# Optimization experiments

Measured on AMD Instinct MI355X. Metric: run time of the kernel, lower is better.

The kernel has to match this reference:

```python
import jax, jax.numpy as jnp
import numpy as np

NEG_SLOPE_GAT = 0.2   # GATConv internal leaky_relu slope (PyG default)
NEG_SLOPE = 0.01      # nn.LeakyReLU default slope


def _gat(h_src_in, h_dst_in, src, dst, Wsrc, Wdst, a_s, a_d, b, n_dst, self_loops):
    """Single-head PyG-style GATConv: gather -> score -> edge softmax -> scatter-sum."""
    hs = h_src_in @ Wsrc            # [N_src, C]
    hd = h_dst_in @ Wdst            # [N_dst, C]
    if self_loops:                  # static flag; same node set on both sides
        loop = jnp.arange(n_dst, dtype=src.dtype)
        src = jnp.concatenate([src, loop])
        dst = jnp.concatenate([dst, loop])
    # attention logits per edge
    e = jax.nn.leaky_relu((hs @ a_s)[src] + (hd @ a_d)[dst], NEG_SLOPE_GAT)  # [E]
    # softmax over edges sharing a destination node
    m = jax.ops.segment_max(e, dst, num_segments=n_dst)
    ex = jnp.exp(e - m[dst])
    denom = jax.ops.segment_sum(ex, dst, num_segments=n_dst)
    alpha = ex / denom[dst]
    out = jax.ops.segment_sum(hs[src] * alpha[:, None], dst, num_segments=n_dst)
    return out + b


def setup_inputs() -> dict:
    key = jax.random.key(0)
    ks = iter(jax.random.split(key, 64))
    NB, NP = 100_000, 50_000
    E_bb, E_pp, E_bp = 800_000, 400_000, 400_000
    FB, FP, H, H2 = 32, 34, 64, 32
    rn = lambda shape, s=0.05: jax.random.normal(next(ks), shape, jnp.float32) * s
    d = {}
    d['x_b'] = rn((NB, FB), 1.0)
    d['x_p'] = rn((NP, FP), 1.0)
    d['ei_bb'] = jax.random.randint(next(ks), (2, E_bb), 0, NB, jnp.int32)
    d['ei_pp'] = jax.random.randint(next(ks), (2, E_pp), 0, NP, jnp.int32)
    d['ei_bp_src'] = jax.random.randint(next(ks), (E_bp,), 0, NB, jnp.int32)
    d['ei_bp_dst'] = jax.random.randint(next(ks), (E_bp,), 0, NP, jnp.int32)
    d['W_in_b'] = rn((FB, H)); d['b_in_b'] = jnp.zeros((H,), jnp.float32)
    d['W_in_p'] = rn((FP, H)); d['b_in_p'] = jnp.zeros((H,), jnp.float32)
    for tag, cin, cout in (('1', H, H), ('2', H, H2)):
        d['W_bb' + tag] = rn((cin, cout)); d['as_bb' + tag] = rn((cout,)); d['ad_bb' + tag] = rn((cout,)); d['b_bb' + tag] = jnp.zeros((cout,), jnp.float32)
        d['W_pp' + tag] = rn((cin, cout)); d['as_pp' + tag] = rn((cout,)); d['ad_pp' + tag] = rn((cout,)); d['b_pp' + tag] = jnp.zeros((cout,), jnp.float32)
        d['Ws_bp' + tag] = rn((cin, cout)); d['Wd_bp' + tag] = rn((cin, cout)); d['as_bp' + tag] = rn((cout,)); d['ad_bp' + tag] = rn((cout,)); d['b_bp' + tag] = jnp.zeros((cout,), jnp.float32)
    d['W_out'] = rn((H2, 1)); d['b_out'] = jnp.zeros((1,), jnp.float32)
    return d


def reference(x_b, x_p, ei_bb, ei_pp, ei_bp_src, ei_bp_dst,
              W_in_b, b_in_b, W_in_p, b_in_p,
              W_bb1, as_bb1, ad_bb1, b_bb1, W_pp1, as_pp1, ad_pp1, b_pp1,
              Ws_bp1, Wd_bp1, as_bp1, ad_bp1, b_bp1,
              W_bb2, as_bb2, ad_bb2, b_bb2, W_pp2, as_pp2, ad_pp2, b_pp2,
              Ws_bp2, Wd_bp2, as_bp2, ad_bp2, b_bp2,
              W_out, b_out):
    NB, NP = x_b.shape[0], x_p.shape[0]
    lr = lambda v: jax.nn.leaky_relu(v, NEG_SLOPE)
    # input projections (dropout is eval-mode identity)
    hb = lr(x_b @ W_in_b + b_in_b)
    hp = lr(x_p @ W_in_p + b_in_p)
    # hetero conv 1 (sum aggregation over relations sharing a dst type)
    ob = _gat(hb, hb, ei_bb[0], ei_bb[1], W_bb1, W_bb1, as_bb1, ad_bb1, b_bb1, NB, True)
    op = (_gat(hp, hp, ei_pp[0], ei_pp[1], W_pp1, W_pp1, as_pp1, ad_pp1, b_pp1, NP, True)
          + _gat(hb, hp, ei_bp_src, ei_bp_dst, Ws_bp1, Wd_bp1, as_bp1, ad_bp1, b_bp1, NP, False))
    hb, hp = lr(ob), lr(op)
    # hetero conv 2
    ob2 = _gat(hb, hb, ei_bb[0], ei_bb[1], W_bb2, W_bb2, as_bb2, ad_bb2, b_bb2, NB, True)
    op2 = (_gat(hp, hp, ei_pp[0], ei_pp[1], W_pp2, W_pp2, as_pp2, ad_pp2, b_pp2, NP, True)
           + _gat(hb, hp, ei_bp_src, ei_bp_dst, Ws_bp2, Wd_bp2, as_bp2, ad_bp2, b_bp2, NP, False))
    hp = lr(op2)
    return hp @ W_out + b_out  # [NP, 1]
```

## Files before the change

kernel.cpp:

```cpp
#include <hip/hip_runtime.h>
#include <hip/hip_bf16.h>
#include <cstdint>
#include <cstddef>


typedef __attribute__((ext_vector_type(8))) short short8;
typedef __attribute__((ext_vector_type(4))) float f32x4;
typedef unsigned int u32;
typedef __hip_bfloat16 bf16;

#define ABITS 9
#define CHUNKE 4096

static __device__ __forceinline__ float b2f(bf16 v) { return __bfloat162float(v); }

static __device__ __forceinline__ float ldf(const void* p, int i, int bf) {
    return bf ? __bfloat162float(((const bf16*)p)[i]) : ((const float*)p)[i];
}

static __device__ __forceinline__ short f2bs(float f) {
    bf16 h = __float2bfloat16(f);
    return *reinterpret_cast<short*>(&h);
}
static __device__ __forceinline__ float bs2f(short s) {
    bf16 h = *reinterpret_cast<bf16*>(&s);
    return __bfloat162float(h);
}
static __device__ __forceinline__ float lo16(u32 u) { return bs2f((short)(u & 0xffffu)); }
static __device__ __forceinline__ float hi16(u32 u) { return bs2f((short)(u >> 16)); }
// ... 16 lines not shown
        c += (e >= 100u && e <= 145u) ? 1 : 0;
    }
    atomicAdd(cnt, c);
    __syncthreads();
    int r = (*cnt > 614) ? 1 : 0;
    __syncthreads();
    return r;
}

__global__ __launch_bounds__(256) void k_fv(
    const unsigned* __restrict__ probe_w, int* __restrict__ flag,
    const void* W_bb1, const void* as_bb1, const void* ad_bb1,
    const void* Ws_bp1, const void* as_bp1,
    const void* W_pp1, const void* as_pp1, const void* ad_pp1,
    const void* Wd_bp1, const void* ad_bp1,
    float* __restrict__ FVg)
{
    __shared__ int cnt;
    int bf = probe_bf(probe_w, &cnt);
    if (threadIdx.x == 0) *flag = bf;
    int lane = threadIdx.x & 63, wv = threadIdx.x >> 6;
    const void* Ws[6] = { W_bb1, W_bb1, Ws_bp1, W_pp1, W_pp1, Wd_bp1 };
    const void* av[6] = { as_bb1, ad_bb1, as_bp1, as_pp1, ad_pp1, ad_bp1 };
#pragma unroll
    for (int v = 0; v < 6; ++v) {
        float a = ldf(av[v], lane, bf);
        for (int k = wv; k < 64; k += 4) {
            float p = ldf(Ws[v], k * 64 + lane, bf) * a;
#pragma unroll
            for (int off = 1; off < 64; off <<= 1) p += __shfl_xor(p, off);
            if (lane == 0) FVg[v * 64 + k] = p;
        }
    }
// ... 77 lines not shown
            vs[r] += __shfl_xor(vs[r], off);
            vd[r] += __shfl_xor(vd[r], off);
            ve[r] += __shfl_xor(ve[r], off);
        }
    int c = lane & 15;
    int row = row0 + quad * 4 + (c & 3);
    if (row < M && c < 12) {
        if (c < 4)       S0[row]  = sel4(vs, c & 3);
        else if (c < 8)  S1v[row] = sel4(vd, c & 3);
        else             S2v[row] = sel4(ve, c & 3);
    }
}

__global__ __launch_bounds__(256) void k_hist_inproj(
    const int* __restrict__ bb_d, const int* __restrict__ pp_d,
    const int* __restrict__ bp_d, int* __restrict__ histM,
    const unsigned* __restrict__ probe_w, int* __restrict__ flag,
    int E_bb, int E_pp, int E_bp, int NB, int NP, int nbkt, int nblk,
    const void* __restrict__ Xb, const void* __restrict__ Wb, const void* __restrict__ Bb,
    bf16* __restrict__ Yb, int MB,
    const void* __restrict__ Xp, const void* __restrict__ Wp, const void* __restrict__ Bp,
    bf16* __restrict__ Yp, int MP,
    const float* __restrict__ FVg,
    float* __restrict__ ss_bb, float* __restrict__ sd_bb, float* __restrict__ ss_bp,
    float* __restrict__ ss_pp, float* __restrict__ sd_pp, float* __restrict__ sd_bp)
{
    __shared__ short WT[64 * 40];
    __shared__ float bl[64];
    __shared__ float FV[192];
    __shared__ int aux[1 << ABITS];
    if ((int)blockIdx.x < nblk) {
        for (int i = threadIdx.x; i < nbkt; i += 256) aux[i] = 0;
        __syncthreads();
        int E_all = E_bb + E_pp + E_bp;
        int base = blockIdx.x * CHUNKE;
        int end = base + CHUNKE < E_all ? base + CHUNKE : E_all;
        for (int i = base + threadIdx.x; i < end; i += 256) {
            int d;
            if (i < E_bb) d = bb_d[i];
            else if (i < E_bb + E_pp) d = NB + pp_d[i - E_bb];
            else d = NB + NP + bp_d[i - E_bb - E_pp];
            atomicAdd(&aux[d >> ABITS], 1);
        }
        __syncthreads();
        for (int i = threadIdx.x; i < nbkt; i += 256)
            histM[(size_t)i * nblk + blockIdx.x] = aux[i];
    } else {
        int bfv = probe_bf(probe_w, &aux[0]);
        int bid = blockIdx.x - nblk;
        int nbb = (MB + 63) >> 6;
        if (bid < nbb)
            in_proj_body<32>(WT, bl, FV, bid, Xb, Wb, Bb, FVg,
                Yb, ss_bb, sd_bb, ss_bp, MB, bfv);
        else
            in_proj_body<34>(WT, bl, FV, bid - nbb, Xp, Wp, Bp, FVg + 192,
                Yp, ss_pp, sd_pp, sd_bp, MP, bfv);
    }
}

__global__ __launch_bounds__(1024) void k_scan1(const int* __restrict__ deg,
                                                int* __restrict__ out,
                                                int* __restrict__ bsum, int n)
{
// ... 41 lines not shown
    if (wid == 0 && lane < 16) {
        int w0 = wsum[lane];
#pragma unroll
        for (int off = 1; off < 16; off <<= 1) {
            int y = __shfl_up(w0, off, 16);
            if (lane >= off) w0 += y;
        }
        wsum[lane] = w0;
    }
    __syncthreads();
    int base = (wid > 0) ? wsum[wid - 1] : 0;
    if (threadIdx.x < nb) bsum[threadIdx.x] = base + x - v;
}

__global__ __launch_bounds__(1024) void k_scan3(int* __restrict__ indptr,
                                                const int* __restrict__ bsum,
                                                int n, int E)
{
    int gid = blockIdx.x * 1024 + threadIdx.x;
    if (gid < n) indptr[gid] += bsum[blockIdx.x];
    if (gid == 0) indptr[n] = E;
}

template <int N1, int N2, bool S1F, bool S2F>
static __device__ __forceinline__ void dual_body(
    short* WT, int bid, const bf16* __restrict__ H,
    const void* __restrict__ W1, const void* __restrict__ W2,
    const void* __restrict__ as1, const void* __restrict__ ad1,
    const void* __restrict__ as2, const void* __restrict__ ad2,
    bf16* __restrict__ HS1, bf16* __restrict__ HS2,
    float* __restrict__ SS1, float* __restrict__ SD1,
    float* __restrict__ SS2, float* __restrict__ SD2,
    int M, int bf)
{
    constexpr int KP = 72;
    constexpr int T1 = N1 / 16, T2 = N2 / 16, T = T1 + T2;
    for (int i = threadIdx.x; i < N1 * 64; i += 256) {
        int n = i >> 6, k = i & 63;
        WT[n * KP + k] = f2bs(ldf(W1, k * N1 + n, bf));
    }
    for (int i = threadIdx.x; i < N2 * 64; i += 256) {
        int n = i >> 6, k = i & 63;
        WT[(N1 + n) * KP + k] = f2bs(ldf(W2, k * N2 + n, bf));
    }
    __syncthreads();

    int lane = threadIdx.x & 63;
    int wv   = threadIdx.x >> 6;
    int m = lane & 15, quad = lane >> 4;
    int row0 = (bid * 4 + wv) * 16;
    if (row0 >= M) return;

    const short* Hs = (const short*)H;
    int arow = row0 + m; if (arow >= M) arow = M - 1;

    f32x4 acc[T] = {};
#pragma unroll
    for (int ks = 0; ks < 2; ++ks) {
        short8 a = *(const short8*)&Hs[(size_t)arow * 64 + ks * 32 + quad * 8];
#pragma unroll
        for (int tt = 0; tt < T; ++tt) {
            short8 bfr = *(const short8*)&WT[((lane & 15) + 16 * tt) * KP + ks * 32 + quad * 8];
            acc[tt] = __builtin_amdgcn_mfma_f32_16x16x32_bf16(a, bfr, acc[tt], 0, 0, 0);
        }
    }

    float vs1[4] = {}, vd1[4] = {}, vs2[4] = {}, vd2[4] = {};
#pragma unroll
    for (int tt = 0; tt < T1; ++tt) {
        int col = (lane & 15) + 16 * tt;
        float av = ldf(as1, col, bf), dv = ldf(ad1, col, bf);
#pragma unroll
        for (int r = 0; r < 4; ++r) {
            vs1[r] += acc[tt][r] * av;
            vd1[r] += acc[tt][r] * dv;
        }
    }
#pragma unroll
    for (int tt = 0; tt < T2; ++tt) {
        int col = (lane & 15) + 16 * tt;
        float av = ldf(as2, col, bf), dv = ldf(ad2, col, bf);
#pragma unroll
        for (int r = 0; r < 4; ++r) {
            vs2[r] += acc[T1 + tt][r] * av;
            vd2[r] += acc[T1 + tt][r] * dv;
        }
    }
#pragma unroll
    for (int off = 1; off < 16; off <<= 1)
#pragma unroll
        for (int r = 0; r < 4; ++r) {
            vs1[r] += __shfl_xor(vs1[r], off);
            vd1[r] += __shfl_xor(vd1[r], off);
            vs2[r] += __shfl_xor(vs2[r], off);
            vd2[r] += __shfl_xor(vd2[r], off);
        }
    int c = lane & 15;
    {
        int row = row0 + quad * 4 + (c & 3);
        if (row < M) {
            if (c < 4)       SS1[row] = sel4(vs1, c & 3);
            else if (c < 8)  SD1[row] = sel4(vd1, c & 3);
            else if (c < 12) SS2[row] = sel4(vs2, c & 3);
            else             SD2[row] = sel4(vd2, c & 3);
        }
    }

    if (S1F) {
#pragma unroll
        for (int tt = 0; tt < T1; ++tt) {
            int col = (lane & 15) + 16 * tt;
#pragma unroll
            for (int r = 0; r < 4; ++r) {
                int row = row0 + quad * 4 + r;
                if (row < M)
                    HS1[(size_t)row * N1 + col] = __float2bfloat16(acc[tt][r]);
            }
        }
    }
    if (S2F) {
#pragma unroll
        for (int tt = 0; tt < T2; ++tt) {
            int col = (lane & 15) + 16 * tt;
#pragma unroll
            for (int r = 0; r < 4; ++r) {
                int row = row0 + quad * 4 + r;
                if (row < M)
                    HS2[(size_t)row * N2 + col] = __float2bfloat16(acc[T1 + tt][r]);
            }
        }
    }
}

template <int N, bool STORE>
static __device__ __forceinline__ void proj_body(
    short* WT, int bid, const bf16* __restrict__ H, const void* __restrict__ W,
    const void* __restrict__ a_s, const void* __restrict__ a_d,
    bf16* __restrict__ HS, float* __restrict__ SS, float* __restrict__ SD,
    int M, int bf)
{
    constexpr int KP = 72;
    constexpr int T = N / 16;
    for (int i = threadIdx.x; i < N * 64; i += 256) {
        int n = i >> 6, k = i & 63;
        WT[n * KP + k] = f2bs(ldf(W, k * N + n, bf));
    }
    __syncthreads();

    int lane = threadIdx.x & 63;
    int wv   = threadIdx.x >> 6;
    int m = lane & 15, quad = lane >> 4;
    int row0 = (bid * 4 + wv) * 16;
    if (row0 >= M) return;

    const short* Hs = (const short*)H;
    int arow = row0 + m; if (arow >= M) arow = M - 1;

    f32x4 acc[T] = {};
#pragma unroll
    for (int ks = 0; ks < 2; ++ks) {
        short8 a = *(const short8*)&Hs[(size_t)arow * 64 + ks * 32 + quad * 8];
#pragma unroll
        for (int tt = 0; tt < T; ++tt) {
            short8 bfr = *(const short8*)&WT[((lane & 15) + 16 * tt) * KP + ks * 32 + quad * 8];
            acc[tt] = __builtin_amdgcn_mfma_f32_16x16x32_bf16(a, bfr, acc[tt], 0, 0, 0);
        }
    }

    float asv[T], adv[T];
#pragma unroll
    for (int tt = 0; tt < T; ++tt) {
        int col = (lane & 15) + 16 * tt;
        asv[tt] = ldf(a_s, col, bf);
        adv[tt] = ldf(a_d, col, bf);
    }
    float vs[4] = {}, vd[4] = {};
#pragma unroll
    for (int tt = 0; tt < T; ++tt)
#pragma unroll
        for (int r = 0; r < 4; ++r) {
            vs[r] += acc[tt][r] * asv[tt];
            vd[r] += acc[tt][r] * adv[tt];
        }
#pragma unroll
    for (int off = 1; off < 16; off <<= 1)
#pragma unroll
        for (int r = 0; r < 4; ++r) {
            vs[r] += __shfl_xor(vs[r], off);
            vd[r] += __shfl_xor(vd[r], off);
        }
    int c = lane & 15;
    if (c < 8) {
        int row = row0 + quad * 4 + (c & 3);
        if (row < M) {
            if (c < 4) SS[row] = sel4(vs, c & 3);
            else       SD[row] = sel4(vd, c & 3);
        }
    }

    if (STORE) {
#pragma unroll
        for (int tt = 0; tt < T; ++tt) {
            int col = (lane & 15) + 16 * tt;
#pragma unroll
            for (int r = 0; r < 4; ++r) {
                int row = row0 + quad * 4 + r;
                if (row < M)
                    HS[(size_t)row * N + col] = __float2bfloat16(acc[tt][r]);
            }
        }
    }
}

__global__ __launch_bounds__(256) void k_scatter(
    const int* __restrict__ bb_s, const int* __restrict__ bb_d,
    const int* __restrict__ pp_s, const int* __restrict__ pp_d,
    const int* __restrict__ bp_s, const int* __restrict__ bp_d,
    const int* __restrict__ histS, unsigned* __restrict__ ebuf,
    int E_bb, int E_pp, int E_bp, int NB, int NP, int nbkt, int nblk)
{
    __shared__ int cur[1 << ABITS];
    for (int i = threadIdx.x; i < nbkt; i += 256)
        cur[i] = histS[(size_t)i * nblk + blockIdx.x];
    __syncthreads();
    int E_all = E_bb + E_pp + E_bp;
    int base = blockIdx.x * CHUNKE;
    int end = base + CHUNKE < E_all ? base + CHUNKE : E_all;
    for (int i = base + threadIdx.x; i < end; i += 256) {
        int s, d;
        if (i < E_bb) { s = bb_s[i]; d = bb_d[i]; }
        else if (i < E_bb + E_pp) { int j = i - E_bb; s = pp_s[j]; d = NB + pp_d[j]; }
        else { int j = i - E_bb - E_pp; s = bp_s[j]; d = NB + NP + bp_d[j]; }
        int p = atomicAdd(&cur[d >> ABITS], 1);
        ebuf[p] = ((unsigned)(d & ((1 << ABITS) - 1)) << 20) | (unsigned)s;
    }
}

__global__ __launch_bounds__(256) void k_finalize(
    const unsigned* __restrict__ ebuf, const int* __restrict__ histS,
    int* __restrict__ ip_all, int2* __restrict__ sw,
    const float* __restrict__ ss_bb, const float* __restrict__ sd_bb,
    const float* __restrict__ ss_pp, const float* __restrict__ sd_pp,
    const float* __restrict__ ss_bp, const float* __restrict__ sd_bp,
    int NB, int NP, int NALL, int E_all, int nbkt, int nblk)
{
    __shared__ int h[1 << ABITS];
    __shared__ int pre[1 << ABITS];
    __shared__ int wq[4];
    int b = blockIdx.x;
    int d0 = b << ABITS;
    int nloc = NALL - d0 < (1 << ABITS) ? NALL - d0 : (1 << ABITS);
    int t = threadIdx.x;
    for (int i = t; i < (1 << ABITS); i += 256) h[i] = 0;
    __syncthreads();
    int s0 = histS[(size_t)b * nblk];
    int s1 = histS[(size_t)(b + 1) * nblk];
    for (int i = s0 + t; i < s1; i += 256)
        atomicAdd(&h[ebuf[i] >> 20], 1);
    __syncthreads();
    int v0 = h[2 * t], v1 = h[2 * t + 1];
    int ps = v0 + v1;
    int lane = t & 63, wid = t >> 6;
    int x = ps;
#pragma unroll
    for (int off = 1; off < 64; off <<= 1) {
        int y = __shfl_up(x, off, 64);
        if (lane >= off) x += y;
    }
    if (lane == 63) wq[wid] = x;
    __syncthreads();
    if (t == 0) {
        int a = 0;
#pragma unroll
        for (int w = 0; w < 4; ++w) { int tmp = wq[w]; wq[w] = a; a += tmp; }
    }
    __syncthreads();
    int excl = wq[wid] + x - ps;
    pre[2 * t]     = excl;
    pre[2 * t + 1] = excl + v0;
    __syncthreads();
    for (int i = t; i < nloc; i += 256) ip_all[d0 + i] = s0 + pre[i];
    if (d0 + nloc == NALL && t == 0) ip_all[NALL] = E_all;
    for (int i = t; i < (1 << ABITS); i += 256) h[i] = s0 + pre[i];
    __syncthreads();
    for (int i = s0 + t; i < s1; i += 256) {
        unsigned e = ebuf[i];
        int dl = (int)(e >> 20);
        int src = (int)(e & 0xFFFFFu);
        int p = atomicAdd(&h[dl], 1);
        int d = d0 + dl;
        float ssv, sdv;
        if (d < NB)           { ssv = ss_bb[src]; sdv = sd_bb[d]; }
        else if (d < NB + NP) { ssv = ss_pp[src]; sdv = sd_pp[d - NB]; }
        else                  { ssv = ss_bp[src]; sdv = sd_bp[d - NB - NP]; }
        int2 pk; pk.x = src; pk.y = __float_as_int(__expf(lrelu2(ssv + sdv)));
        sw[p] = pk;
    }
}

static __device__ __forceinline__ void gather1_body(
    int bid, const int* __restrict__ ip, const int2* __restrict__ sw,
    const float* __restrict__ SS, const float* __restrict__ SD,
    const bf16* __restrict__ HS, bf16* __restrict__ OUT, int M)
{
    int lane = threadIdx.x & 63;
    int half = lane >> 5, hl = lane & 31;
    int d = bid * 4 + (threadIdx.x >> 6);
    if (d >= M) return;
    const u32* H32 = (const u32*)HS;
    float ax = 0.f, ay = 0.f, den = 0.f;
// ... 104 lines not shown
    const float* __restrict__ ss_bb, const float* __restrict__ sd_bb,
    const bf16* __restrict__ hb, bf16* __restrict__ agg_bb, int NB,
    const int* __restrict__ ip_pp, const int* __restrict__ ip_bp,
    const float* __restrict__ ss_pp, const float* __restrict__ sd_pp,
    const bf16* __restrict__ hp,
    bf16* __restrict__ agg_pp, bf16* __restrict__ agg_bp, int NP)
{
    int nbb = (NB + 3) >> 2;
    if ((int)blockIdx.x < nbb)
        gather1_body(blockIdx.x, ip_bb, sw, ss_bb, sd_bb, hb, agg_bb, NB);
    else
        gather2_body(blockIdx.x - nbb, ip_pp, sw, ss_pp, sd_pp, hp,
                     ip_bp, hb, agg_pp, agg_bp, NP);
}

template <bool DUAL>
static __device__ __forceinline__ void postproj_body(
    short* WT, float* bl, int bid,
    const bf16* __restrict__ A1, const bf16* __restrict__ A2,
    const void* __restrict__ W1, const void* __restrict__ W2,
    const void* __restrict__ B1, const void* __restrict__ B2,
    bf16* __restrict__ OUT, int M, int bf)
{
    constexpr int KP = 72;
    for (int i = threadIdx.x; i < 64 * 64; i += 256) {
        int n = i >> 6, k = i & 63;
        WT[n * KP + k] = f2bs(ldf(W1, k * 64 + n, bf));
        if (DUAL) WT[(64 + n) * KP + k] = f2bs(ldf(W2, k * 64 + n, bf));
    }
    if (threadIdx.x < 64) {
        float b = ldf(B1, threadIdx.x, bf);
        if (DUAL) b += ldf(B2, threadIdx.x, bf);
        bl[threadIdx.x] = b;
    }
    __syncthreads();

    int lane = threadIdx.x & 63;
    int wv   = threadIdx.x >> 6;
    int m = lane & 15, quad = lane >> 4;
    int row0 = (bid * 4 + wv) * 16;
    if (row0 >= M) return;

    const short* A1s = (const short*)A1;
    const short* A2s = (const short*)A2;
    int arow = row0 + m; if (arow >= M) arow = M - 1;

    f32x4 acc[4] = {};
#pragma unroll
    for (int ks = 0; ks < 2; ++ks) {
        short8 a1 = *(const short8*)&A1s[(size_t)arow * 64 + ks * 32 + quad * 8];
#pragma unroll
        for (int tt = 0; tt < 4; ++tt) {
            short8 bfr = *(const short8*)&WT[((lane & 15) + 16 * tt) * KP + ks * 32 + quad * 8];
            acc[tt] = __builtin_amdgcn_mfma_f32_16x16x32_bf16(a1, bfr, acc[tt], 0, 0, 0);
        }
        if (DUAL) {
            short8 a2 = *(const short8*)&A2s[(size_t)arow * 64 + ks * 32 + quad * 8];
#pragma unroll
            for (int tt = 0; tt < 4; ++tt) {
                short8 bfr = *(const short8*)&WT[(64 + (lane & 15) + 16 * tt) * KP + ks * 32 + quad * 8];
                acc[tt] = __builtin_amdgcn_mfma_f32_16x16x32_bf16(a2, bfr, acc[tt], 0, 0, 0);
            }
        }
    }

#pragma unroll
    for (int tt = 0; tt < 4; ++tt) {
        int col = (lane & 15) + 16 * tt;
        float bb = bl[col];
#pragma unroll
        for (int r = 0; r < 4; ++r) {
            int row = row0 + quad * 4 + r;
            if (row < M) {
                float v = acc[tt][r] + bb;
                v = v > 0.f ? v : 0.01f * v;
                OUT[(size_t)row * 64 + col] = __float2bfloat16(v);
            }
        }
    }
}

__global__ __launch_bounds__(256) void k_postproj1(
    const bf16* __restrict__ agg_pp, const bf16* __restrict__ agg_bp,
    const void* W_pp1, const void* Ws_bp1,
    const void* b_pp1, const void* b_bp1, bf16* __restrict__ hp2, int MP,
    const bf16* __restrict__ agg_bb, const void* W_bb1, const void* b_bb1,
    bf16* __restrict__ hb2, int MB, const int* __restrict__ flag)
{
    const int bf = *flag;
    __shared__ short WT[128 * 72];
    __shared__ float bl[64];
    int npb = (MP + 63) >> 6;
    if ((int)blockIdx.x < npb)
        postproj_body<true>(WT, bl, blockIdx.x, agg_pp, agg_bp,
                            W_pp1, Ws_bp1, b_pp1, b_bp1, hp2, MP, bf);
    else
        postproj_body<false>(WT, bl, blockIdx.x - npb, agg_bb, nullptr,
                             W_bb1, nullptr, b_bb1, nullptr, hb2, MB, bf);
}

__global__ __launch_bounds__(256) void k_proj2_all(
    const bf16* __restrict__ hp2,
    const void* W_pp2, const void* Wd_bp2,
    const void* as_pp2, const void* ad_pp2, const void* as_bp2, const void* ad_bp2,
    bf16* hs2_pp, float* ss2_pp, float* sd2_pp, float* junkNP, float* sd2_bp, int MP,
    const bf16* __restrict__ hb2,
    const void* Ws_bp2, bf16* hs2_bp, float* ss2_bp, float* junkNB, int MB,
    const int* __restrict__ flag)
{
    const int bf = *flag;
    __shared__ short WT[64 * 72];
    int npb = (MP + 63) >> 6;
    if ((int)blockIdx.x < npb)
        dual_body<32, 32, true, false>(WT, blockIdx.x, hp2, W_pp2, Wd_bp2,
            as_pp2, ad_pp2, as_bp2, ad_bp2, hs2_pp, nullptr,
            ss2_pp, sd2_pp, junkNP, sd2_bp, MP, bf);
    else
        proj_body<32, true>(WT, blockIdx.x - npb, hb2, Ws_bp2,
            as_bp2, ad_bp2, hs2_bp, ss2_bp, junkNB, MB, bf);
}

__global__ __launch_bounds__(256) void k_gather_out(
    const int* __restrict__ ip1, const int2* __restrict__ sw,
    const float* __restrict__ SS1, const float* __restrict__ SD1,
    const bf16* __restrict__ HS1,
    const int* __restrict__ ip2,
    const float* __restrict__ SS2, const float* __restrict__ SD2,
    const bf16* __restrict__ HS2,
    const void* __restrict__ b1, const void* __restrict__ b2,
    const void* __restrict__ Wout, const void* __restrict__ bout,
    void* __restrict__ OUT, int M, const int* __restrict__ flag)
{
    const int bf = *flag;
    int lane = threadIdx.x & 63;
// ... 84 lines not shown
    const void *W_pp2 = d_in[27], *as_pp2 = d_in[28], *ad_pp2 = d_in[29], *b_pp2 = d_in[30];
    const void *Ws_bp2 = d_in[31], *Wd_bp2 = d_in[32], *as_bp2 = d_in[33], *ad_bp2 = d_in[34], *b_bp2 = d_in[35];
    const void *W_out = d_in[36], *b_out = d_in[37];

    const int NB   = in_sizes[0] / 32;
    const int NP   = in_sizes[1] / 34;
    const int E_bb = in_sizes[2] / 2;
    const int E_pp = in_sizes[3] / 2;
    const int E_bp = in_sizes[4];
    const int E_all = E_bb + E_pp + E_bp;
    const int NALL  = NB + 2 * NP;
    const int* bb_s = ei_bb;  const int* bb_d = ei_bb + E_bb;
    const int* pp_s = ei_pp;  const int* pp_d = ei_pp + E_pp;
    (void)ws_size; (void)n_in; (void)out_size;

    const int nbkt  = (NALL + (1 << ABITS) - 1) >> ABITS;
    const int nblk  = (E_all + CHUNKE - 1) / CHUNKE;
    const int nh    = nbkt * nblk;

    char* base = (char*)d_ws;
    size_t o = 0;
    auto alloc = [&](size_t bytes) { char* p = base + o; o += (bytes + 255) & ~(size_t)255; return p; };

    int* flag  = (int*)alloc(256);
    float* FVg = (float*)alloc(6 * 64 * 4);
    int* bsum  = (int*)alloc(1024 * 4);
    int* histM = (int*)alloc((size_t)nh * 4);
    int* histS = (int*)alloc((size_t)(nh + 1) * 4);
    int* ip_all = (int*)alloc((size_t)(NALL + 1) * 4);
    unsigned* ebuf = (unsigned*)alloc((size_t)E_all * 4);
    int2* sw = (int2*)alloc((size_t)E_all * 8);
    float* ss_bb = (float*)alloc((size_t)NB * 4);
    float* sd_bb = (float*)alloc((size_t)NB * 4);
    float* ss_bp = (float*)alloc((size_t)NB * 4);
    float* ss_pp = (float*)alloc((size_t)NP * 4);
    float* sd_pp = (float*)alloc((size_t)NP * 4);
    float* sd_bp = (float*)alloc((size_t)NP * 4);
    float* junkNB = (float*)alloc((size_t)NB * 4);
    float* junkNP = (float*)alloc((size_t)NP * 4);
    float* ss2_bp = ss_bb;
    float* ss2_pp = ss_pp;
    float* sd2_pp = sd_pp;
    float* sd2_bp = sd_bp;

    char* S1 = alloc((size_t)NB * 64 * 2);
    char* S2 = alloc((size_t)NP * 64 * 2);
    char* S3 = alloc((size_t)NB * 64 * 2);
    char* S4 = alloc((size_t)NB * 64 * 2);
    char* S5 = alloc((size_t)NB * 64 * 2);
    char* S6 = alloc((size_t)NP * 64 * 2);

    bf16* hb     = (bf16*)S1;
    bf16* hp     = (bf16*)S2;
    bf16* agg_bb = (bf16*)S3;
    bf16* hb2    = (bf16*)S4;
    bf16* agg_bp = (bf16*)S5;
    bf16* agg_pp = (bf16*)S6;
    bf16* hp2    = (bf16*)S2;
    bf16* hs2_pp = (bf16*)S3;
    bf16* hs2_bp = (bf16*)S1;

    auto cdiv = [](int a, int b) { return (a + b - 1) / b; };

    const int* ip_bb = ip_all;
    const int* ip_pp = ip_all + NB;
    const int* ip_bp = ip_all + NB + NP;

    k_fv<<<1, 256, 0, stream>>>(
        (const unsigned*)x_b, flag,
        W_bb1, as_bb1, ad_bb1, Ws_bp1, as_bp1,
        W_pp1, as_pp1, ad_pp1, Wd_bp1, ad_bp1, FVg);

    k_hist_inproj<<<nblk + cdiv(NB, 64) + cdiv(NP, 64), 256, 0, stream>>>(
        bb_d, pp_d, bp_d, histM, (const unsigned*)x_b, flag,
        E_bb, E_pp, E_bp, NB, NP, nbkt, nblk,
        x_b, W_in_b, b_in_b, hb, NB, x_p, W_in_p, b_in_p, hp, NP,
        FVg, ss_bb, sd_bb, ss_bp, ss_pp, sd_pp, sd_bp);

    int sb1 = cdiv(nh, 1024);
    k_scan1<<<sb1, 1024, 0, stream>>>(histM, histS, bsum, nh);
    k_scan2<<<1, 1024, 0, stream>>>(bsum, sb1);
    k_scan3<<<sb1, 1024, 0, stream>>>(histS, bsum, nh, E_all);

    k_scatter<<<nblk, 256, 0, stream>>>(
        bb_s, bb_d, pp_s, pp_d, bp_s, bp_d, histS, ebuf,
        E_bb, E_pp, E_bp, NB, NP, nbkt, nblk);

    k_finalize<<<nbkt, 256, 0, stream>>>(ebuf, histS, ip_all, sw,
                                         ss_bb, sd_bb, ss_pp, sd_pp, ss_bp, sd_bp,
                                         NB, NP, NALL, E_all, nbkt, nblk);

    k_gather12<<<cdiv(NB, 4) + cdiv(NP, 4), 256, 0, stream>>>(
        ip_bb, sw, ss_bb, sd_bb, hb, agg_bb, NB,
        ip_pp, ip_bp, ss_pp, sd_pp, hp, agg_pp, agg_bp, NP);

    k_postproj1<<<cdiv(NP, 64) + cdiv(NB, 64), 256, 0, stream>>>(
        agg_pp, agg_bp, W_pp1, Ws_bp1, b_pp1, b_bp1, hp2, NP,
        agg_bb, W_bb1, b_bb1, hb2, NB, flag);

    k_proj2_all<<<cdiv(NP, 64) + cdiv(NB, 64), 256, 0, stream>>>(
        hp2, W_pp2, Wd_bp2, as_pp2, ad_pp2, as_bp2, ad_bp2,
        hs2_pp, ss2_pp, sd2_pp, junkNP, sd2_bp, NP,
        hb2, Ws_bp2, hs2_bp, ss2_bp, junkNB, NB, flag);

    k_gather_out<<<cdiv(NP, 4), 256, 0, stream>>>(
        ip_pp, sw, ss2_pp, sd2_pp, hs2_pp,
        ip_bp, ss2_bp, sd2_bp, hs2_bp,
        b_pp2, b_bp2, W_out, b_out, d_out, NP, flag);
}
```

Baseline: 429.8 us.

## Replace bucketed CSR build with per-node degree atomics; fuse layer-1 post and layer-2 projections

```diff
diff --git a/kernel.cpp b/kernel.cpp
--- a/kernel.cpp
+++ b/kernel.cpp
@@ -9,10 +9,7 @@
 typedef unsigned int u32;
 typedef __hip_bfloat16 bf16;
 
-#define ABITS 9
 #define CHUNKE 4096
-
-static __device__ __forceinline__ float b2f(bf16 v) { return __bfloat162float(v); }
 
 static __device__ __forceinline__ float ldf(const void* p, int i, int bf) {
     return bf ? __bfloat162float(((const bf16*)p)[i]) : ((const float*)p)[i];
@@ -59,9 +56,15 @@
     const void* Ws_bp1, const void* as_bp1,
     const void* W_pp1, const void* as_pp1, const void* ad_pp1,
     const void* Wd_bp1, const void* ad_bp1,
-    float* __restrict__ FVg)
+    float* __restrict__ FVg, int* __restrict__ deg, int NALL)
 {
     __shared__ int cnt;
+    if (blockIdx.x > 0) {
+        int stride = ((int)gridDim.x - 1) * 256;
+        for (int i = ((int)blockIdx.x - 1) * 256 + threadIdx.x; i < NALL; i += stride)
+            deg[i] = 0;
+        return;
+    }
     int bf = probe_bf(probe_w, &cnt);
     if (threadIdx.x == 0) *flag = bf;
     int lane = threadIdx.x & 63, wv = threadIdx.x >> 6;
@@ -169,9 +172,9 @@
 
 __global__ __launch_bounds__(256) void k_hist_inproj(
     const int* __restrict__ bb_d, const int* __restrict__ pp_d,
-    const int* __restrict__ bp_d, int* __restrict__ histM,
-    const unsigned* __restrict__ probe_w, int* __restrict__ flag,
-    int E_bb, int E_pp, int E_bp, int NB, int NP, int nbkt, int nblk,
+    const int* __restrict__ bp_d, int* __restrict__ deg,
+    const unsigned* __restrict__ probe_w,
+    int E_bb, int E_pp, int E_bp, int NB, int NP, int nblk,
     const void* __restrict__ Xb, const void* __restrict__ Wb, const void* __restrict__ Bb,
     bf16* __restrict__ Yb, int MB,
     const void* __restrict__ Xp, const void* __restrict__ Wp, const void* __restrict__ Bp,
@@ -183,10 +186,8 @@
     __shared__ short WT[64 * 40];
     __shared__ float bl[64];
     __shared__ float FV[192];
-    __shared__ int aux[1 << ABITS];
+    __shared__ int cnt;
     if ((int)blockIdx.x < nblk) {
-        for (int i = threadIdx.x; i < nbkt; i += 256) aux[i] = 0;
-        __syncthreads();
         int E_all = E_bb + E_pp + E_bp;
         int base = blockIdx.x * CHUNKE;
         int end = base + CHUNKE < E_all ? base + CHUNKE : E_all;
@@ -195,13 +196,10 @@
             if (i < E_bb) d = bb_d[i];
             else if (i < E_bb + E_pp) d = NB + pp_d[i - E_bb];
             else d = NB + NP + bp_d[i - E_bb - E_pp];
-            atomicAdd(&aux[d >> ABITS], 1);
-        }
-        __syncthreads();
-        for (int i = threadIdx.x; i < nbkt; i += 256)
-            histM[(size_t)i * nblk + blockIdx.x] = aux[i];
+            atomicAdd(&deg[d], 1);
+        }
     } else {
-        int bfv = probe_bf(probe_w, &aux[0]);
+        int bfv = probe_bf(probe_w, &cnt);
         int bid = blockIdx.x - nblk;
         int nbb = (MB + 63) >> 6;
         if (bid < nbb)
@@ -273,286 +271,46 @@
 }
 
 __global__ __launch_bounds__(1024) void k_scan3(int* __restrict__ indptr,
+                                                int* __restrict__ cur,
                                                 const int* __restrict__ bsum,
                                                 int n, int E)
 {
     int gid = blockIdx.x * 1024 + threadIdx.x;
-    if (gid < n) indptr[gid] += bsum[blockIdx.x];
+    if (gid < n) {
+        int v = indptr[gid] + bsum[blockIdx.x];
+        indptr[gid] = v;
+        cur[gid] = v;
+    }
     if (gid == 0) indptr[n] = E;
 }
 
-template <int N1, int N2, bool S1F, bool S2F>
-static __device__ __forceinline__ void dual_body(
-    short* WT, int bid, const bf16* __restrict__ H,
-    const void* __restrict__ W1, const void* __restrict__ W2,
-    const void* __restrict__ as1, const void* __restrict__ ad1,
-    const void* __restrict__ as2, const void* __restrict__ ad2,
-    bf16* __restrict__ HS1, bf16* __restrict__ HS2,
-    float* __restrict__ SS1, float* __restrict__ SD1,
-    float* __restrict__ SS2, float* __restrict__ SD2,
-    int M, int bf)
-{
-    constexpr int KP = 72;
-    constexpr int T1 = N1 / 16, T2 = N2 / 16, T = T1 + T2;
-    for (int i = threadIdx.x; i < N1 * 64; i += 256) {
-        int n = i >> 6, k = i & 63;
-        WT[n * KP + k] = f2bs(ldf(W1, k * N1 + n, bf));
-    }
-    for (int i = threadIdx.x; i < N2 * 64; i += 256) {
-        int n = i >> 6, k = i & 63;
-        WT[(N1 + n) * KP + k] = f2bs(ldf(W2, k * N2 + n, bf));
-    }
-    __syncthreads();
-
-    int lane = threadIdx.x & 63;
-    int wv   = threadIdx.x >> 6;
-    int m = lane & 15, quad = lane >> 4;
-    int row0 = (bid * 4 + wv) * 16;
-    if (row0 >= M) return;
-
-    const short* Hs = (const short*)H;
-    int arow = row0 + m; if (arow >= M) arow = M - 1;
-
-    f32x4 acc[T] = {};
-#pragma unroll
-    for (int ks = 0; ks < 2; ++ks) {
-        short8 a = *(const short8*)&Hs[(size_t)arow * 64 + ks * 32 + quad * 8];
-#pragma unroll
-        for (int tt = 0; tt < T; ++tt) {
-            short8 bfr = *(const short8*)&WT[((lane & 15) + 16 * tt) * KP + ks * 32 + quad * 8];
-            acc[tt] = __builtin_amdgcn_mfma_f32_16x16x32_bf16(a, bfr, acc[tt], 0, 0, 0);
-        }
-    }
-
-    float vs1[4] = {}, vd1[4] = {}, vs2[4] = {}, vd2[4] = {};
-#pragma unroll
-    for (int tt = 0; tt < T1; ++tt) {
-        int col = (lane & 15) + 16 * tt;
-        float av = ldf(as1, col, bf), dv = ldf(ad1, col, bf);
-#pragma unroll
-        for (int r = 0; r < 4; ++r) {
-            vs1[r] += acc[tt][r] * av;
-            vd1[r] += acc[tt][r] * dv;
-        }
-    }
-#pragma unroll
-    for (int tt = 0; tt < T2; ++tt) {
-        int col = (lane & 15) + 16 * tt;
-        float av = ldf(as2, col, bf), dv = ldf(ad2, col, bf);
-#pragma unroll
-        for (int r = 0; r < 4; ++r) {
-            vs2[r] += acc[T1 + tt][r] * av;
-            vd2[r] += acc[T1 + tt][r] * dv;
-        }
-    }
-#pragma unroll
-    for (int off = 1; off < 16; off <<= 1)
-#pragma unroll
-        for (int r = 0; r < 4; ++r) {
-            vs1[r] += __shfl_xor(vs1[r], off);
-            vd1[r] += __shfl_xor(vd1[r], off);
-            vs2[r] += __shfl_xor(vs2[r], off);
-            vd2[r] += __shfl_xor(vd2[r], off);
-        }
-    int c = lane & 15;
-    {
-        int row = row0 + quad * 4 + (c & 3);
-        if (row < M) {
-            if (c < 4)       SS1[row] = sel4(vs1, c & 3);
-            else if (c < 8)  SD1[row] = sel4(vd1, c & 3);
-            else if (c < 12) SS2[row] = sel4(vs2, c & 3);
-            else             SD2[row] = sel4(vd2, c & 3);
-        }
-    }
-
-    if (S1F) {
-#pragma unroll
-        for (int tt = 0; tt < T1; ++tt) {
-            int col = (lane & 15) + 16 * tt;
-#pragma unroll
-            for (int r = 0; r < 4; ++r) {
-                int row = row0 + quad * 4 + r;
-                if (row < M)
-                    HS1[(size_t)row * N1 + col] = __float2bfloat16(acc[tt][r]);
-            }
-        }
-    }
-    if (S2F) {
-#pragma unroll
-        for (int tt = 0; tt < T2; ++tt) {
-            int col = (lane & 15) + 16 * tt;
-#pragma unroll
-            for (int r = 0; r < 4; ++r) {
-                int row = row0 + quad * 4 + r;
-                if (row < M)
-                    HS2[(size_t)row * N2 + col] = __float2bfloat16(acc[T1 + tt][r]);
-            }
-        }
-    }
-}
-
-template <int N, bool STORE>
-static __device__ __forceinline__ void proj_body(
-    short* WT, int bid, const bf16* __restrict__ H, const void* __restrict__ W,
-    const void* __restrict__ a_s, const void* __restrict__ a_d,
-    bf16* __restrict__ HS, float* __restrict__ SS, float* __restrict__ SD,
-    int M, int bf)
-{
-    constexpr int KP = 72;
-    constexpr int T = N / 16;
-    for (int i = threadIdx.x; i < N * 64; i += 256) {
-        int n = i >> 6, k = i & 63;
-        WT[n * KP + k] = f2bs(ldf(W, k * N + n, bf));
-    }
-    __syncthreads();
-
-    int lane = threadIdx.x & 63;
-    int wv   = threadIdx.x >> 6;
-    int m = lane & 15, quad = lane >> 4;
-    int row0 = (bid * 4 + wv) * 16;
-    if (row0 >= M) return;
-
-    const short* Hs = (const short*)H;
-    int arow = row0 + m; if (arow >= M) arow = M - 1;
-
-    f32x4 acc[T] = {};
-#pragma unroll
-    for (int ks = 0; ks < 2; ++ks) {
-        short8 a = *(const short8*)&Hs[(size_t)arow * 64 + ks * 32 + quad * 8];
-#pragma unroll
-        for (int tt = 0; tt < T; ++tt) {
-            short8 bfr = *(const short8*)&WT[((lane & 15) + 16 * tt) * KP + ks * 32 + quad * 8];
-            acc[tt] = __builtin_amdgcn_mfma_f32_16x16x32_bf16(a, bfr, acc[tt], 0, 0, 0);
-        }
-    }
-
-    float asv[T], adv[T];
-#pragma unroll
-    for (int tt = 0; tt < T; ++tt) {
-        int col = (lane & 15) + 16 * tt;
-        asv[tt] = ldf(a_s, col, bf);
-        adv[tt] = ldf(a_d, col, bf);
-    }
-    float vs[4] = {}, vd[4] = {};
-#pragma unroll
-    for (int tt = 0; tt < T; ++tt)
-#pragma unroll
-        for (int r = 0; r < 4; ++r) {
-            vs[r] += acc[tt][r] * asv[tt];
-            vd[r] += acc[tt][r] * adv[tt];
-        }
-#pragma unroll
-    for (int off = 1; off < 16; off <<= 1)
-#pragma unroll
-        for (int r = 0; r < 4; ++r) {
-            vs[r] += __shfl_xor(vs[r], off);
-            vd[r] += __shfl_xor(vd[r], off);
-        }
-    int c = lane & 15;
-    if (c < 8) {
-        int row = row0 + quad * 4 + (c & 3);
-        if (row < M) {
-            if (c < 4) SS[row] = sel4(vs, c & 3);
-            else       SD[row] = sel4(vd, c & 3);
-        }
-    }
-
-    if (STORE) {
-#pragma unroll
-        for (int tt = 0; tt < T; ++tt) {
-            int col = (lane & 15) + 16 * tt;
-#pragma unroll
-            for (int r = 0; r < 4; ++r) {
-                int row = row0 + quad * 4 + r;
-                if (row < M)
-                    HS[(size_t)row * N + col] = __float2bfloat16(acc[tt][r]);
-            }
-        }
-    }
-}
-
-__global__ __launch_bounds__(256) void k_scatter(
+__global__ __launch_bounds__(256) void k_scatter2(
     const int* __restrict__ bb_s, const int* __restrict__ bb_d,
     const int* __restrict__ pp_s, const int* __restrict__ pp_d,
     const int* __restrict__ bp_s, const int* __restrict__ bp_d,
-    const int* __restrict__ histS, unsigned* __restrict__ ebuf,
-    int E_bb, int E_pp, int E_bp, int NB, int NP, int nbkt, int nblk)
-{
-    __shared__ int cur[1 << ABITS];
-    for (int i = threadIdx.x; i < nbkt; i += 256)
-        cur[i] = histS[(size_t)i * nblk + blockIdx.x];
-    __syncthreads();
+    const float* __restrict__ ss_bb, const float* __restrict__ sd_bb,
+    const float* __restrict__ ss_pp, const float* __restrict__ sd_pp,
+    const float* __restrict__ ss_bp, const float* __restrict__ sd_bp,
+    int* __restrict__ cur, int2* __restrict__ sw,
+    int E_bb, int E_pp, int E_bp, int NB, int NP)
+{
     int E_all = E_bb + E_pp + E_bp;
     int base = blockIdx.x * CHUNKE;
     int end = base + CHUNKE < E_all ? base + CHUNKE : E_all;
     for (int i = base + threadIdx.x; i < end; i += 256) {
-        int s, d;
-        if (i < E_bb) { s = bb_s[i]; d = bb_d[i]; }
-        else if (i < E_bb + E_pp) { int j = i - E_bb; s = pp_s[j]; d = NB + pp_d[j]; }
-        else { int j = i - E_bb - E_pp; s = bp_s[j]; d = NB + NP + bp_d[j]; }
-        int p = atomicAdd(&cur[d >> ABITS], 1);
-        ebuf[p] = ((unsigned)(d & ((1 << ABITS) - 1)) << 20) | (unsigned)s;
-    }
-}
-
-__global__ __launch_bounds__(256) void k_finalize(
-    const unsigned* __restrict__ ebuf, const int* __restrict__ histS,
-    int* __restrict__ ip_all, int2* __restrict__ sw,
-    const float* __restrict__ ss_bb, const float* __restrict__ sd_bb,
-    const float* __restrict__ ss_pp, const float* __restrict__ sd_pp,
-    const float* __restrict__ ss_bp, const float* __restrict__ sd_bp,
-    int NB, int NP, int NALL, int E_all, int nbkt, int nblk)
-{
-    __shared__ int h[1 << ABITS];
-    __shared__ int pre[1 << ABITS];
-    __shared__ int wq[4];
-    int b = blockIdx.x;
-    int d0 = b << ABITS;
-    int nloc = NALL - d0 < (1 << ABITS) ? NALL - d0 : (1 << ABITS);
-    int t = threadIdx.x;
-    for (int i = t; i < (1 << ABITS); i += 256) h[i] = 0;
-    __syncthreads();
-    int s0 = histS[(size_t)b * nblk];
-    int s1 = histS[(size_t)(b + 1) * nblk];
-    for (int i = s0 + t; i < s1; i += 256)
-        atomicAdd(&h[ebuf[i] >> 20], 1);
-    __syncthreads();
-    int v0 = h[2 * t], v1 = h[2 * t + 1];
-    int ps = v0 + v1;
-    int lane = t & 63, wid = t >> 6;
-    int x = ps;
-#pragma unroll
-    for (int off = 1; off < 64; off <<= 1) {
-        int y = __shfl_up(x, off, 64);
-        if (lane >= off) x += y;
-    }
-    if (lane == 63) wq[wid] = x;
-    __syncthreads();
-    if (t == 0) {
-        int a = 0;
-#pragma unroll
-        for (int w = 0; w < 4; ++w) { int tmp = wq[w]; wq[w] = a; a += tmp; }
-    }
-    __syncthreads();
-    int excl = wq[wid] + x - ps;
-    pre[2 * t]     = excl;
-    pre[2 * t + 1] = excl + v0;
-    __syncthreads();
-    for (int i = t; i < nloc; i += 256) ip_all[d0 + i] = s0 + pre[i];
-    if (d0 + nloc == NALL && t == 0) ip_all[NALL] = E_all;
-    for (int i = t; i < (1 << ABITS); i += 256) h[i] = s0 + pre[i];
-    __syncthreads();
-    for (int i = s0 + t; i < s1; i += 256) {
-        unsigned e = ebuf[i];
-        int dl = (int)(e >> 20);
-        int src = (int)(e & 0xFFFFFu);
-        int p = atomicAdd(&h[dl], 1);
-        int d = d0 + dl;
-        float ssv, sdv;
-        if (d < NB)           { ssv = ss_bb[src]; sdv = sd_bb[d]; }
-        else if (d < NB + NP) { ssv = ss_pp[src]; sdv = sd_pp[d - NB]; }
-        else                  { ssv = ss_bp[src]; sdv = sd_bp[d - NB - NP]; }
-        int2 pk; pk.x = src; pk.y = __float_as_int(__expf(lrelu2(ssv + sdv)));
+        int s, dg; float ssv, sdv;
+        if (i < E_bb) {
+            s = bb_s[i]; int d = bb_d[i]; dg = d;
+            ssv = ss_bb[s]; sdv = sd_bb[d];
+        } else if (i < E_bb + E_pp) {
+            int j = i - E_bb; s = pp_s[j]; int d = pp_d[j]; dg = NB + d;
+            ssv = ss_pp[s]; sdv = sd_pp[d];
+        } else {
+            int j = i - E_bb - E_pp; s = bp_s[j]; int d = bp_d[j]; dg = NB + NP + d;
+            ssv = ss_bp[s]; sdv = sd_bp[d];
+        }
+        int p = atomicAdd(&cur[dg], 1);
+        int2 pk; pk.x = s; pk.y = __float_as_int(__expf(lrelu2(ssv + sdv)));
         sw[p] = pk;
     }
 }
@@ -687,23 +445,31 @@
                      ip_bp, hb, agg_pp, agg_bp, NP);
 }
 
-template <bool DUAL>
-static __device__ __forceinline__ void postproj_body(
-    short* WT, float* bl, int bid,
+template <bool D1, bool D2>
+static __device__ __forceinline__ void fused_body(
+    short* WT1, short* WT2, short* HT, float* bl, int bid,
     const bf16* __restrict__ A1, const bf16* __restrict__ A2,
-    const void* __restrict__ W1, const void* __restrict__ W2,
-    const void* __restrict__ B1, const void* __restrict__ B2,
-    bf16* __restrict__ OUT, int M, int bf)
+    const void* W1a, const void* W1b, const void* B1a, const void* B1b,
+    const void* W2a, const void* W2b,
+    const void* av0, const void* av1, const void* av2,
+    bf16* __restrict__ HS,
+    float* __restrict__ S0, float* __restrict__ S1v, float* __restrict__ S2v,
+    int M, int bf)
 {
     constexpr int KP = 72;
     for (int i = threadIdx.x; i < 64 * 64; i += 256) {
         int n = i >> 6, k = i & 63;
-        WT[n * KP + k] = f2bs(ldf(W1, k * 64 + n, bf));
-        if (DUAL) WT[(64 + n) * KP + k] = f2bs(ldf(W2, k * 64 + n, bf));
+        WT1[n * KP + k] = f2bs(ldf(W1a, k * 64 + n, bf));
+        if (D1) WT1[(64 + n) * KP + k] = f2bs(ldf(W1b, k * 64 + n, bf));
+    }
+    for (int i = threadIdx.x; i < 32 * 64; i += 256) {
+        int n = i >> 6, k = i & 63;
+        WT2[n * KP + k] = f2bs(ldf(W2a, k * 32 + n, bf));
+        if (D2) WT2[(32 + n) * KP + k] = f2bs(ldf(W2b, k * 32 + n, bf));
     }
     if (threadIdx.x < 64) {
-        float b = ldf(B1, threadIdx.x, bf);
-        if (DUAL) b += ldf(B2, threadIdx.x, bf);
+        float b = ldf(B1a, threadIdx.x, bf);
+        if (D1) b += ldf(B1b, threadIdx.x, bf);
         bl[threadIdx.x] = b;
     }
     __syncthreads();
@@ -712,85 +478,138 @@
     int wv   = threadIdx.x >> 6;
     int m = lane & 15, quad = lane >> 4;
     int row0 = (bid * 4 + wv) * 16;
-    if (row0 >= M) return;
+    bool act = row0 < M;
 
     const short* A1s = (const short*)A1;
     const short* A2s = (const short*)A2;
-    int arow = row0 + m; if (arow >= M) arow = M - 1;
-
-    f32x4 acc[4] = {};
-#pragma unroll
-    for (int ks = 0; ks < 2; ++ks) {
-        short8 a1 = *(const short8*)&A1s[(size_t)arow * 64 + ks * 32 + quad * 8];
+    if (act) {
+        int arow = row0 + m; if (arow >= M) arow = M - 1;
+        f32x4 acc[4] = {};
+#pragma unroll
+        for (int ks = 0; ks < 2; ++ks) {
+            short8 a1 = *(const short8*)&A1s[(size_t)arow * 64 + ks * 32 + quad * 8];
+#pragma unroll
+            for (int tt = 0; tt < 4; ++tt) {
+                short8 bfr = *(const short8*)&WT1[((lane & 15) + 16 * tt) * KP + ks * 32 + quad * 8];
+                acc[tt] = __builtin_amdgcn_mfma_f32_16x16x32_bf16(a1, bfr, acc[tt], 0, 0, 0);
+            }
+            if (D1) {
+                short8 a2 = *(const short8*)&A2s[(size_t)arow * 64 + ks * 32 + quad * 8];
+#pragma unroll
+                for (int tt = 0; tt < 4; ++tt) {
+                    short8 bfr = *(const short8*)&WT1[(64 + (lane & 15) + 16 * tt) * KP + ks * 32 + quad * 8];
+                    acc[tt] = __builtin_amdgcn_mfma_f32_16x16x32_bf16(a2, bfr, acc[tt], 0, 0, 0);
+                }
+            }
+        }
 #pragma unroll
         for (int tt = 0; tt < 4; ++tt) {
-            short8 bfr = *(const short8*)&WT[((lane & 15) + 16 * tt) * KP + ks * 32 + quad * 8];
-            acc[tt] = __builtin_amdgcn_mfma_f32_16x16x32_bf16(a1, bfr, acc[tt], 0, 0, 0);
-        }
-        if (DUAL) {
-            short8 a2 = *(const short8*)&A2s[(size_t)arow * 64 + ks * 32 + quad * 8];
-#pragma unroll
-            for (int tt = 0; tt < 4; ++tt) {
-                short8 bfr = *(const short8*)&WT[(64 + (lane & 15) + 16 * tt) * KP + ks * 32 + quad * 8];
-                acc[tt] = __builtin_amdgcn_mfma_f32_16x16x32_bf16(a2, bfr, acc[tt], 0, 0, 0);
-            }
-        }
-    }
-
-#pragma unroll
-    for (int tt = 0; tt < 4; ++tt) {
-        int col = (lane & 15) + 16 * tt;
-        float bb = bl[col];
-#pragma unroll
-        for (int r = 0; r < 4; ++r) {
-            int row = row0 + quad * 4 + r;
-            if (row < M) {
+            int col = (lane & 15) + 16 * tt;
+            float bb = bl[col];
+#pragma unroll
+            for (int r = 0; r < 4; ++r) {
                 float v = acc[tt][r] + bb;
                 v = v > 0.f ? v : 0.01f * v;
-                OUT[(size_t)row * 64 + col] = __float2bfloat16(v);
+                HT[(wv * 16 + quad * 4 + r) * 80 + col] = f2bs(v);
             }
         }
     }
-}
-
-__global__ __launch_bounds__(256) void k_postproj1(
+    __syncthreads();
+
+    f32x4 acc2[D2 ? 4 : 2] = {};
+    if (act) {
+        int arow = row0 + m; if (arow >= M) arow = M - 1;
+        int al = arow - bid * 64;
+#pragma unroll
+        for (int ks = 0; ks < 2; ++ks) {
+            short8 a = *(const short8*)&HT[al * 80 + ks * 32 + quad * 8];
+#pragma unroll
+            for (int tt = 0; tt < (D2 ? 4 : 2); ++tt) {
+                short8 bfr = *(const short8*)&WT2[((lane & 15) + 16 * tt) * KP + ks * 32 + quad * 8];
+                acc2[tt] = __builtin_amdgcn_mfma_f32_16x16x32_bf16(a, bfr, acc2[tt], 0, 0, 0);
+            }
+        }
+    }
+
+    float vs[4] = {}, vd[4] = {}, ve[4] = {};
+#pragma unroll
+    for (int tt = 0; tt < 2; ++tt) {
+        int col = (lane & 15) + 16 * tt;
+        float a0 = ldf(av0, col, bf);
+#pragma unroll
+        for (int r = 0; r < 4; ++r) vs[r] += acc2[tt][r] * a0;
+        if (D1) {
+            float a1 = ldf(av1, col, bf);
+#pragma unroll
+            for (int r = 0; r < 4; ++r) vd[r] += acc2[tt][r] * a1;
+        }
+    }
+    if (D2) {
+#pragma unroll
+        for (int tt = 0; tt < 2; ++tt) {
+            int col = (lane & 15) + 16 * tt;
+            float a2 = ldf(av2, col, bf);
+#pragma unroll
+            for (int r = 0; r < 4; ++r) ve[r] += acc2[2 + tt][r] * a2;
+        }
+    }
+#pragma unroll
+    for (int off = 1; off < 16; off <<= 1)
+#pragma unroll
+        for (int r = 0; r < 4; ++r) {
+            vs[r] += __shfl_xor(vs[r], off);
+            if (D1) vd[r] += __shfl_xor(vd[r], off);
+            if (D2) ve[r] += __shfl_xor(ve[r], off);
+        }
+    int c = lane & 15;
+    int row = row0 + quad * 4 + (c & 3);
+    if (act && row < M) {
+        if (c < 4)                    S0[row]  = sel4(vs, c & 3);
+        else if (D1 && c < 8)         S1v[row] = sel4(vd, c & 3);
+        else if (D2 && c >= 8 && c < 12) S2v[row] = sel4(ve, c & 3);
+    }
+    if (act) {
+#pragma unroll
+        for (int tt = 0; tt < 2; ++tt) {
+            int col = (lane & 15) + 16 * tt;
+#pragma unroll
+            for (int r = 0; r < 4; ++r) {
+                int row2 = row0 + quad * 4 + r;
+                if (row2 < M)
+                    HS[(size_t)row2 * 32 + col] = __float2bfloat16(acc2[tt][r]);
+            }
+        }
+    }
+}
+
+__global__ __launch_bounds__(256) void k_fused_proj(
     const bf16* __restrict__ agg_pp, const bf16* __restrict__ agg_bp,
-    const void* W_pp1, const void* Ws_bp1,
-    const void* b_pp1, const void* b_bp1, bf16* __restrict__ hp2, int MP,
+    const void* W_pp1, const void* Ws_bp1, const void* b_pp1, const void* b_bp1,
+    const void* W_pp2, const void* Wd_bp2,
+    const void* as_pp2, const void* ad_pp2, const void* ad_bp2,
+    bf16* __restrict__ hs2_pp, float* __restrict__ ss2_pp,
+    float* __restrict__ sd2_pp, float* __restrict__ sd2_bp, int MP,
     const bf16* __restrict__ agg_bb, const void* W_bb1, const void* b_bb1,
-    bf16* __restrict__ hb2, int MB, const int* __restrict__ flag)
+    const void* Ws_bp2, const void* as_bp2,
+    bf16* __restrict__ hs2_bp, float* __restrict__ ss2_bp, int MB,
+    const int* __restrict__ flag)
 {
     const int bf = *flag;
-    __shared__ short WT[128 * 72];
+    __shared__ __align__(16) short WT1[128 * 72];
+    __shared__ __align__(16) short WT2[64 * 72];
+    __shared__ __align__(16) short HT[64 * 80];
     __shared__ float bl[64];
     int npb = (MP + 63) >> 6;
     if ((int)blockIdx.x < npb)
-        postproj_body<true>(WT, bl, blockIdx.x, agg_pp, agg_bp,
-                            W_pp1, Ws_bp1, b_pp1, b_bp1, hp2, MP, bf);
+        fused_body<true, true>(WT1, WT2, HT, bl, blockIdx.x,
+            agg_pp, agg_bp, W_pp1, Ws_bp1, b_pp1, b_bp1,
+            W_pp2, Wd_bp2, as_pp2, ad_pp2, ad_bp2,
+            hs2_pp, ss2_pp, sd2_pp, sd2_bp, MP, bf);
     else
-        postproj_body<false>(WT, bl, blockIdx.x - npb, agg_bb, nullptr,
-                             W_bb1, nullptr, b_bb1, nullptr, hb2, MB, bf);
-}
-
-__global__ __launch_bounds__(256) void k_proj2_all(
-    const bf16* __restrict__ hp2,
-    const void* W_pp2, const void* Wd_bp2,
-    const void* as_pp2, const void* ad_pp2, const void* as_bp2, const void* ad_bp2,
-    bf16* hs2_pp, float* ss2_pp, float* sd2_pp, float* junkNP, float* sd2_bp, int MP,
-    const bf16* __restrict__ hb2,
-    const void* Ws_bp2, bf16* hs2_bp, float* ss2_bp, float* junkNB, int MB,
-    const int* __restrict__ flag)
-{
-    const int bf = *flag;
-    __shared__ short WT[64 * 72];
-    int npb = (MP + 63) >> 6;
-    if ((int)blockIdx.x < npb)
-        dual_body<32, 32, true, false>(WT, blockIdx.x, hp2, W_pp2, Wd_bp2,
-            as_pp2, ad_pp2, as_bp2, ad_bp2, hs2_pp, nullptr,
-            ss2_pp, sd2_pp, junkNP, sd2_bp, MP, bf);
-    else
-        proj_body<32, true>(WT, blockIdx.x - npb, hb2, Ws_bp2,
-            as_bp2, ad_bp2, hs2_bp, ss2_bp, junkNB, MB, bf);
+        fused_body<false, false>(WT1, WT2, HT, bl, blockIdx.x - npb,
+            agg_bb, nullptr, W_bb1, nullptr, b_bb1, nullptr,
+            Ws_bp2, nullptr, as_bp2, nullptr, nullptr,
+            hs2_bp, ss2_bp, nullptr, nullptr, MB, bf);
 }
 
 __global__ __launch_bounds__(256) void k_gather_out(
@@ -905,9 +724,7 @@
     const int* pp_s = ei_pp;  const int* pp_d = ei_pp + E_pp;
     (void)ws_size; (void)n_in; (void)out_size;
 
-    const int nbkt  = (NALL + (1 << ABITS) - 1) >> ABITS;
     const int nblk  = (E_all + CHUNKE - 1) / CHUNKE;
-    const int nh    = nbkt * nblk;
 
     char* base = (char*)d_ws;
     size_t o = 0;
@@ -916,10 +733,9 @@
     int* flag  = (int*)alloc(256);
     float* FVg = (float*)alloc(6 * 64 * 4);
     int* bsum  = (int*)alloc(1024 * 4);
-    int* histM = (int*)alloc((size_t)nh * 4);
-    int* histS = (int*)alloc((size_t)(nh + 1) * 4);
+    int* deg   = (int*)alloc((size_t)NALL * 4);
+    int* cur   = (int*)alloc((size_t)NALL * 4);
     int* ip_all = (int*)alloc((size_t)(NALL + 1) * 4);
-    unsigned* ebuf = (unsigned*)alloc((size_t)E_all * 4);
     int2* sw = (int2*)alloc((size_t)E_all * 8);
     float* ss_bb = (float*)alloc((size_t)NB * 4);
     float* sd_bb = (float*)alloc((size_t)NB * 4);
@@ -927,8 +743,6 @@
     float* ss_pp = (float*)alloc((size_t)NP * 4);
     float* sd_pp = (float*)alloc((size_t)NP * 4);
     float* sd_bp = (float*)alloc((size_t)NP * 4);
-    float* junkNB = (float*)alloc((size_t)NB * 4);
-    float* junkNP = (float*)alloc((size_t)NP * 4);
     float* ss2_bp = ss_bb;
     float* ss2_pp = ss_pp;
     float* sd2_pp = sd_pp;
@@ -937,18 +751,15 @@
     char* S1 = alloc((size_t)NB * 64 * 2);
     char* S2 = alloc((size_t)NP * 64 * 2);
     char* S3 = alloc((size_t)NB * 64 * 2);
-    char* S4 = alloc((size_t)NB * 64 * 2);
-    char* S5 = alloc((size_t)NB * 64 * 2);
+    char* S5 = alloc((size_t)NP * 64 * 2);
     char* S6 = alloc((size_t)NP * 64 * 2);
 
     bf16* hb     = (bf16*)S1;
     bf16* hp     = (bf16*)S2;
     bf16* agg_bb = (bf16*)S3;
-    bf16* hb2    = (bf16*)S4;
     bf16* agg_bp = (bf16*)S5;
     bf16* agg_pp = (bf16*)S6;
-    bf16* hp2    = (bf16*)S2;
-    bf16* hs2_pp = (bf16*)S3;
+    bf16* hs2_pp = (bf16*)S2;
     bf16* hs2_bp = (bf16*)S1;
 
     auto cdiv = [](int a, int b) { return (a + b - 1) / b; };
@@ -957,42 +768,37 @@
     const int* ip_pp = ip_all + NB;
     const int* ip_bp = ip_all + NB + NP;
 
-    k_fv<<<1, 256, 0, stream>>>(
+    k_fv<<<1 + 64, 256, 0, stream>>>(
         (const unsigned*)x_b, flag,
         W_bb1, as_bb1, ad_bb1, Ws_bp1, as_bp1,
-        W_pp1, as_pp1, ad_pp1, Wd_bp1, ad_bp1, FVg);
+        W_pp1, as_pp1, ad_pp1, Wd_bp1, ad_bp1, FVg, deg, NALL);
 
     k_hist_inproj<<<nblk + cdiv(NB, 64) + cdiv(NP, 64), 256, 0, stream>>>(
-        bb_d, pp_d, bp_d, histM, (const unsigned*)x_b, flag,
-        E_bb, E_pp, E_bp, NB, NP, nbkt, nblk,
+        bb_d, pp_d, bp_d, deg, (const unsigned*)x_b,
+        E_bb, E_pp, E_bp, NB, NP, nblk,
         x_b, W_in_b, b_in_b, hb, NB, x_p, W_in_p, b_in_p, hp, NP,
         FVg, ss_bb, sd_bb, ss_bp, ss_pp, sd_pp, sd_bp);
 
-    int sb1 = cdiv(nh, 1024);
-    k_scan1<<<sb1, 1024, 0, stream>>>(histM, histS, bsum, nh);
+    int sb1 = cdiv(NALL, 1024);
+    k_scan1<<<sb1, 1024, 0, stream>>>(deg, ip_all, bsum, NALL);
     k_scan2<<<1, 1024, 0, stream>>>(bsum, sb1);
-    k_scan3<<<sb1, 1024, 0, stream>>>(histS, bsum, nh, E_all);
-
-    k_scatter<<<nblk, 256, 0, stream>>>(
-        bb_s, bb_d, pp_s, pp_d, bp_s, bp_d, histS, ebuf,
-        E_bb, E_pp, E_bp, NB, NP, nbkt, nblk);
-
-    k_finalize<<<nbkt, 256, 0, stream>>>(ebuf, histS, ip_all, sw,
-                                         ss_bb, sd_bb, ss_pp, sd_pp, ss_bp, sd_bp,
-                                         NB, NP, NALL, E_all, nbkt, nblk);
+    k_scan3<<<sb1, 1024, 0, stream>>>(ip_all, cur, bsum, NALL, E_all);
+
+    k_scatter2<<<nblk, 256, 0, stream>>>(
+        bb_s, bb_d, pp_s, pp_d, bp_s, bp_d,
+        ss_bb, sd_bb, ss_pp, sd_pp, ss_bp, sd_bp,
+        cur, sw, E_bb, E_pp, E_bp, NB, NP);
 
     k_gather12<<<cdiv(NB, 4) + cdiv(NP, 4), 256, 0, stream>>>(
         ip_bb, sw, ss_bb, sd_bb, hb, agg_bb, NB,
         ip_pp, ip_bp, ss_pp, sd_pp, hp, agg_pp, agg_bp, NP);
 
-    k_postproj1<<<cdiv(NP, 64) + cdiv(NB, 64), 256, 0, stream>>>(
-        agg_pp, agg_bp, W_pp1, Ws_bp1, b_pp1, b_bp1, hp2, NP,
-        agg_bb, W_bb1, b_bb1, hb2, NB, flag);
-
-    k_proj2_all<<<cdiv(NP, 64) + cdiv(NB, 64), 256, 0, stream>>>(
-        hp2, W_pp2, Wd_bp2, as_pp2, ad_pp2, as_bp2, ad_bp2,
-        hs2_pp, ss2_pp, sd2_pp, junkNP, sd2_bp, NP,
-        hb2, Ws_bp2, hs2_bp, ss2_bp, junkNB, NB, flag);
+    k_fused_proj<<<cdiv(NP, 64) + cdiv(NB, 64), 256, 0, stream>>>(
+        agg_pp, agg_bp, W_pp1, Ws_bp1, b_pp1, b_bp1,
+        W_pp2, Wd_bp2, as_pp2, ad_pp2, ad_bp2,
+        hs2_pp, ss2_pp, sd2_pp, sd2_bp, NP,
+        agg_bb, W_bb1, b_bb1, Ws_bp2, as_bp2,
+        hs2_bp, ss2_bp, NB, flag);
 
     k_gather_out<<<cdiv(NP, 4), 256, 0, stream>>>(
         ip_pp, sw, ss2_pp, sd2_pp, hs2_pp,
```

Result: slower. 511.8 us (+19.1%).
